# Performance work log

Measured on AMD Instinct MI355X. Metric: run time of the kernel, lower is better.

## Reference

```python
import itertools
import jax, jax.numpy as jnp
import numpy as np
from jax import lax

B, RES, C = 2048, 7, 512
N = RES * RES            # 49 tokens per window
HEADS = 4
KD = C // 16             # key_dim = 32
D = 4 * KD               # value dim = 128 == C // HEADS
KS = 5                   # dw-conv kernel
EPS = 1e-5


def _bias_idxs():
    pts = list(itertools.product(range(RES), range(RES)))
    offs, idxs = {}, []
    for p1 in pts:
        for p2 in pts:
            o = (abs(p1[0] - p2[0]), abs(p1[1] - p2[1]))
            if o not in offs:
                offs[o] = len(offs)
            idxs.append(offs[o])
    return np.array(idxs, np.int32).reshape(N, N), len(offs)


def setup_inputs() -> dict:
    key = jax.random.key(0)
    k = jax.random.split(key, 20)
    f = jnp.float32
    idxs, noff = _bias_idxs()  # noff == 49 for resolution 7
    qo = 2 * KD + D  # per-head qkv output channels = 192
    return {
        "x": jax.random.normal(k[0], (B, N, C), f),
        "qkv_w": jax.random.normal(k[1], (HEADS, qo, C // HEADS), f) * 0.05,
        "qkv_g": jnp.ones((HEADS, qo), f) + 0.1 * jax.random.normal(k[2], (HEADS, qo), f),
        "qkv_b": 0.1 * jax.random.normal(k[3], (HEADS, qo), f),
        "qkv_m": 0.1 * jax.random.normal(k[4], (HEADS, qo), f),
        "qkv_v": jax.random.uniform(k[5], (HEADS, qo), f, 0.5, 1.5),
        "dw_w": jax.random.normal(k[6], (HEADS, KD, 1, KS, KS), f) * 0.05,
        "dw_g": jnp.ones((HEADS, KD), f) + 0.1 * jax.random.normal(k[7], (HEADS, KD), f),
        "dw_b": 0.1 * jax.random.normal(k[8], (HEADS, KD), f),
        "dw_m": 0.1 * jax.random.normal(k[9], (HEADS, KD), f),
        "dw_v": jax.random.uniform(k[10], (HEADS, KD), f, 0.5, 1.5),
        "proj_w": jax.random.normal(k[11], (C, HEADS * D), f) * 0.05,
        "proj_g": jnp.ones((C,), f) + 0.1 * jax.random.normal(k[12], (C,), f),
        "proj_b": 0.1 * jax.random.normal(k[13], (C,), f),
        "proj_m": 0.1 * jax.random.normal(k[14], (C,), f),
        "proj_v": jax.random.uniform(k[15], (C,), f, 0.5, 1.5),
        "attn_bias": 0.1 * jax.random.normal(k[16], (HEADS, noff), f),
        "bias_idxs": jnp.asarray(idxs),
    }


def _bn(y, g, b, m, v):
    # inference-mode BatchNorm folded as per-channel affine (channels last)
    return (y - m) * (g * jax.lax.rsqrt(v + EPS)) + b


def reference(x, qkv_w, qkv_g, qkv_b, qkv_m, qkv_v,
              dw_w, dw_g, dw_b, dw_m, dw_v,
              proj_w, proj_g, proj_b, proj_m, proj_v,
              attn_bias, bias_idxs):
    scale = KD ** -0.5
    ab = attn_bias[:, bias_idxs]               # [HEADS, N, N] relative-position bias
    chunks = jnp.split(x, HEADS, axis=-1)      # per-head input chunks [B, N, C/HEADS]
    feat = chunks[0]
    outs = []
    for i in range(HEADS):
        if i > 0:
            feat = feat + chunks[i]            # cascade: prev head output + next chunk
        y = jnp.einsum('bnc,oc->bno', feat, qkv_w[i])
        y = _bn(y, qkv_g[i], qkv_b[i], qkv_m[i], qkv_v[i])   # [B, N, 192]
        q, k, v = y[..., :KD], y[..., KD:2 * KD], y[..., 2 * KD:]
        # depthwise 5x5 conv on q over the 7x7 window
        qi = q.reshape(B, RES, RES, KD)
        w = jnp.transpose(dw_w[i], (2, 3, 1, 0))  # OIHW(groups) -> HWIO [5,5,1,KD]
        qi = lax.conv_general_dilated(qi, w, (1, 1), 'SAME',
                                      feature_group_count=KD,
                                      dimension_numbers=('NHWC', 'HWIO', 'NHWC'))
        qi = _bn(qi, dw_g[i], dw_b[i], dw_m[i], dw_v[i])
        q = qi.reshape(B, N, KD)
        attn = jnp.einsum('bnk,bmk->bnm', q, k) * scale + ab[i]  # [B, N, N]
        attn = jax.nn.softmax(attn, axis=-1)
        feat = jnp.einsum('bnm,bmd->bnd', attn, v)               # [B, N, D]
        outs.append(feat)
    h = jax.nn.relu(jnp.concatenate(outs, axis=-1))              # [B, N, HEADS*D]
    out = jnp.einsum('bnd,od->bno', h, proj_w)
    out = _bn(out, proj_g, proj_b, proj_m, proj_v)               # [B, N, C]
    return out
```

## Files before the change

### kernel.cpp

```cpp
#include <hip/hip_runtime.h>
#include <hip/hip_bf16.h>

#define BATCH 2048
#define RES   7
#define NPOS  49
#define CDIM  512
#define HEADS 4
#define KD    32
#define DDIM  128
#define QO    192
#define EPS   1e-5f

#define FSTR 132
#define QSTR 36
#define ASTR 68
#define VSTR 72

#define OFF_QCV  0
#define OFF_ATT  7056
#define OFF_QBUF 25872
#define OFF_KBUF 32928
#define OFF_VTH  39984
#define OFF_VTL  58416
#define SMEM_SZ  76848

typedef __attribute__((ext_vector_type(8))) short short8;
typedef __attribute__((ext_vector_type(4))) float floatx4;

union S8u { short8 v; __hip_bfloat162 h[4]; };
union BU  { __hip_bfloat16 b; unsigned short u; };

__device__ inline short8 pack_bf16x8(float4 a, float4 b) {
    S8u u;
    u.h[0] = __float22bfloat162_rn(make_float2(a.x, a.y));
    u.h[1] = __float22bfloat162_rn(make_float2(a.z, a.w));
    u.h[2] = __float22bfloat162_rn(make_float2(b.x, b.y));
    u.h[3] = __float22bfloat162_rn(make_float2(b.z, b.w));
    return u.v;
}

__device__ inline void split_pack8(float4 a, float4 b, short8& hi, short8& lo) {
    S8u H, L;
    float v0[8] = {a.x, a.y, a.z, a.w, b.x, b.y, b.z, b.w};
    #pragma unroll
    for (int p = 0; p < 4; ++p) {
        __hip_bfloat162 hp = __float22bfloat162_rn(make_float2(v0[2*p], v0[2*p+1]));
        float h0 = __bfloat162float(hp.x);
        float h1 = __bfloat162float(hp.y);
        H.h[p] = hp;
        L.h[p] = __float22bfloat162_rn(make_float2(v0[2*p] - h0, v0[2*p+1] - h1));
    }
    hi = H.v; lo = L.v;
}

#define MFMA(a, b, c) __builtin_amdgcn_mfma_f32_16x16x32_bf16((a), (b), (c), 0, 0, 0)

__global__ __launch_bounds__(512, 2) void fused_cga_kernel(
    const float* __restrict__ x,
    const float* __restrict__ qkv_w,
    const float* __restrict__ qkv_g,  const float* __restrict__ qkv_bb,
    const float* __restrict__ qkv_m,  const float* __restrict__ qkv_v,
    const float* __restrict__ dw_w,
    const float* __restrict__ dw_g,   const float* __restrict__ dw_bb,
    const float* __restrict__ dw_m,   const float* __restrict__ dw_v,
    const float* __restrict__ proj_w,
    const float* __restrict__ proj_g, const float* __restrict__ proj_bb,
    const float* __restrict__ proj_m, const float* __restrict__ proj_v,
    const float* __restrict__ attn_bias,
    const int*   __restrict__ bias_idxs,
    float* __restrict__ out)
{
    __shared__ __align__(16) unsigned char smem[SMEM_SZ];
    float* feat = (float*)smem;
    float* qcv  = (float*)(smem + OFF_QCV);
    float* att  = (float*)(smem + OFF_ATT);
    float* qbuf = (float*)(smem + OFF_QBUF);
    float* kbuf = (float*)(smem + OFF_KBUF);
    unsigned short* vTh = (unsigned short*)(smem + OFF_VTH);
    unsigned short* vTl = (unsigned short*)(smem + OFF_VTL);

    const int b    = blockIdx.x;
    const int tid  = threadIdx.x;
    const int lane = tid & 63;
    const int wid  = tid >> 6;
    const int quad = lane >> 4;
    const int l15  = lane & 15;
    const int mt   = wid & 3;
    const int nh   = wid >> 2;

    const float* xb = x + (size_t)b * NPOS * CDIM;

    floatx4 po[16];
    #pragma unroll
    for (int t = 0; t < 16; ++t) po[t] = (floatx4){0.f, 0.f, 0.f, 0.f};

    for (int i = tid; i < 128 * 15; i += 512) {
        int d = i / 15, c = 49 + (i - d * 15);
        vTh[d * VSTR + c] = 0;
        vTl[d * VSTR + c] = 0;
    }

    for (int head = 0; head < HEADS; ++head) {
        for (int i = tid; i < NPOS * (DDIM / 4); i += 512) {
            int n = i >> 5, c4 = i & 31;
            float4 xv = *(const float4*)(xb + n * CDIM + head * DDIM + c4 * 4);
            float* fp = feat + n * FSTR + c4 * 4;
            if (head == 0) { *(float4*)fp = xv; }
            else {
                float4 f = *(float4*)fp;
                f.x += xv.x; f.y += xv.y; f.z += xv.z; f.w += xv.w;
                *(float4*)fp = f;
            }
        }
        __syncthreads();

        {
            floatx4 qa[6];
            #pragma unroll
            for (int t = 0; t < 6; ++t) qa[t] = (floatx4){0.f, 0.f, 0.f, 0.f};
            for (int ks = 0; ks < 4; ++ks) {
                const float* ap = feat + (mt * 16 + l15) * FSTR + ks * 32 + quad * 8;
                short8 ah, al;
                split_pack8(*(const float4*)ap, *(const float4*)(ap + 4), ah, al);
                #pragma unroll
                for (int t = 0; t < 6; ++t) {
                    const float* wp = qkv_w
                        + (size_t)(head * QO + nh * 96 + t * 16 + l15) * DDIM + ks * 32 + quad * 8;
                    short8 bh, bl;
                    split_pack8(*(const float4*)wp, *(const float4*)(wp + 4), bh, bl);
                    qa[t] = MFMA(ah, bh, qa[t]);
                    qa[t] = MFMA(al, bh, qa[t]);
                    qa[t] = MFMA(ah, bl, qa[t]);
                }
            }
            #pragma unroll
            for (int t = 0; t < 6; ++t) {
                int o   = nh * 96 + t * 16 + l15;
                int idx = head * QO + o;
                float s  = qkv_g[idx] * rsqrtf(qkv_v[idx] + EPS);
                float tt = qkv_bb[idx] - qkv_m[idx] * s;
                #pragma unroll
                for (int r = 0; r < 4; ++r) {
                    int row = mt * 16 + quad * 4 + r;
                    if (row < NPOS) {
                        float y = qa[t][r] * s + tt;
                        if (o < KD)          qbuf[row * QSTR + o] = y;
                        else if (o < 2 * KD) kbuf[row * QSTR + (o - KD)] = y;
                        else {
                            int d = o - 2 * KD;
                            BU hu, lu;
                            __hip_bfloat162 hp = __float22bfloat162_rn(make_float2(y, 0.f));
                            hu.b = hp.x;
                            float hf = __bfloat162float(hp.x);
                            __hip_bfloat162 lp = __float22bfloat162_rn(make_float2(y - hf, 0.f));
                            lu.b = lp.x;
                            vTh[d * VSTR + row] = hu.u;
                            vTl[d * VSTR + row] = lu.u;
                        }
                    }
                }
            }
        }
        __syncthreads();

        for (int i = tid; i < NPOS * KD; i += 512) {
            int n = i >> 5, ch = i & 31;
            int rr = n / RES, cc = n - rr * RES;
            const float* wd = dw_w + (size_t)(head * KD + ch) * 25;
            float acc = 0.f;
            #pragma unroll
            for (int dy = 0; dy < 5; ++dy) {
                int ry = rr + dy - 2;
                if (ry < 0 || ry >= RES) continue;
                #pragma unroll
                for (int dx = 0; dx < 5; ++dx) {
                    int cx = cc + dx - 2;
                    if (cx < 0 || cx >= RES) continue;
                    acc += qbuf[(ry * RES + cx) * QSTR + ch] * wd[dy * 5 + dx];
                }
            }
            int idx = head * KD + ch;
            float s  = dw_g[idx] * rsqrtf(dw_v[idx] + EPS);
            float tt = dw_bb[idx] - dw_m[idx] * s;
            qcv[n * QSTR + ch] = acc * s + tt;
        }
        __syncthreads();

        {
            floatx4 sa[2];
            sa[0] = (floatx4){0.f, 0.f, 0.f, 0.f};
            sa[1] = (floatx4){0.f, 0.f, 0.f, 0.f};
            const float* ap = qcv + (mt * 16 + l15) * QSTR + quad * 8;
            short8 ah, al;
            split_pack8(*(const float4*)ap, *(const float4*)(ap + 4), ah, al);
            #pragma unroll
            for (int t = 0; t < 2; ++t) {
                const float* kp = kbuf + ((nh * 2 + t) * 16 + l15) * QSTR + quad * 8;
                short8 bh, bl;
                split_pack8(*(const float4*)kp, *(const float4*)(kp + 4), bh, bl);
                sa[t] = MFMA(ah, bh, sa[t]);
                sa[t] = MFMA(al, bh, sa[t]);
                sa[t] = MFMA(ah, bl, sa[t]);
            }
            const float scale = 0.17677669529663687f;
            #pragma unroll
            for (int t = 0; t < 2; ++t) {
                int nn = (nh * 2 + t) * 16 + l15;
                #pragma unroll
                for (int r = 0; r < 4; ++r) {
                    int row = mt * 16 + quad * 4 + r;
                    if (row < NPOS) {
                        if (nn < NPOS)
                            att[row * ASTR + nn] = sa[t][r] * scale
                                + attn_bias[head * NPOS + bias_idxs[row * NPOS + nn]];
                        else
                            att[row * ASTR + nn] = 0.f;
                    }
                }
            }
        }
        __syncthreads();

        {
            int row = tid >> 3, g = tid & 7;
            if (row < NPOS) {
                float mx = -1e30f;
                for (int n = g; n < NPOS; n += 8) mx = fmaxf(mx, att[row * ASTR + n]);
                #pragma unroll
                for (int d = 1; d < 8; d <<= 1) mx = fmaxf(mx, __shfl_xor(mx, d));
                float sm = 0.f;
                for (int n = g; n < NPOS; n += 8) {
                    float e = __expf(att[row * ASTR + n] - mx);
                    att[row * ASTR + n] = e;
                    sm += e;
                }
                #pragma unroll
                for (int d = 1; d < 8; d <<= 1) sm += __shfl_xor(sm, d);
                float inv = 1.f / sm;
                for (int n = g; n < NPOS; n += 8) att[row * ASTR + n] *= inv;
            }
        }
        __syncthreads();

        {
            short8 ah[2], al[2];
            #pragma unroll
            for (int ks = 0; ks < 2; ++ks) {
                const float* ap = att + (mt * 16 + l15) * ASTR + ks * 32 + quad * 8;
                split_pack8(*(const float4*)ap, *(const float4*)(ap + 4), ah[ks], al[ks]);
            }
            __syncthreads();
            floatx4 pa[4];
            #pragma unroll
            for (int t = 0; t < 4; ++t) pa[t] = (floatx4){0.f, 0.f, 0.f, 0.f};
            #pragma unroll
            for (int ks = 0; ks < 2; ++ks) {
                #pragma unroll
                for (int t = 0; t < 4; ++t) {
                    int off = ((nh * 4 + t) * 16 + l15) * VSTR + ks * 32 + quad * 8;
                    short8 bh = *(const short8*)(vTh + off);
                    short8 bl = *(const short8*)(vTl + off);
                    pa[t] = MFMA(ah[ks], bh, pa[t]);
                    pa[t] = MFMA(al[ks], bh, pa[t]);
                    pa[t] = MFMA(ah[ks], bl, pa[t]);
                }
            }
            #pragma unroll
            for (int t = 0; t < 4; ++t) {
                int d = (nh * 4 + t) * 16 + l15;
                #pragma unroll
                for (int r = 0; r < 4; ++r) {
                    int row = mt * 16 + quad * 4 + r;
                    if (row < NPOS) feat[row * FSTR + d] = pa[t][r];
                }
            }
        }
        __syncthreads();

        {
            const int nbase = wid * 64;
            for (int ks = 0; ks < 4; ++ks) {
                short8 af[4];
                #pragma unroll
                for (int mm = 0; mm < 4; ++mm) {
                    const float* ap = feat + (mm * 16 + l15) * FSTR + ks * 32 + quad * 8;
                    float4 a0 = *(const float4*)ap;
                    float4 a1 = *(const float4*)(ap + 4);
                    a0.x = fmaxf(a0.x, 0.f); a0.y = fmaxf(a0.y, 0.f);
                    a0.z = fmaxf(a0.z, 0.f); a0.w = fmaxf(a0.w, 0.f);
                    a1.x = fmaxf(a1.x, 0.f); a1.y = fmaxf(a1.y, 0.f);
                    a1.z = fmaxf(a1.z, 0.f); a1.w = fmaxf(a1.w, 0.f);
                    af[mm] = pack_bf16x8(a0, a1);
                }
                #pragma unroll
                for (int j = 0; j < 4; ++j) {
                    const float* wp = proj_w
                        + (size_t)(nbase + j * 16 + l15) * CDIM + head * DDIM + ks * 32 + quad * 8;
                    short8 bf = pack_bf16x8(*(const float4*)wp, *(const float4*)(wp + 4));
                    #pragma unroll
                    for (int mm = 0; mm < 4; ++mm)
                        po[mm * 4 + j] = MFMA(af[mm], bf, po[mm * 4 + j]);
                }
            }
        }
        __syncthreads();
    }

    {
        const int nbase = wid * 64;
        #pragma unroll
        for (int j = 0; j < 4; ++j) {
            int o = nbase + j * 16 + l15;
            float s  = proj_g[o] * rsqrtf(proj_v[o] + EPS);
            float tt = proj_bb[o] - proj_m[o] * s;
            #pragma unroll
            for (int mm = 0; mm < 4; ++mm) {
                #pragma unroll
                for (int r = 0; r < 4; ++r) {
                    int row = mm * 16 + quad * 4 + r;
                    if (row < NPOS)
                        out[((size_t)b * NPOS + row) * CDIM + o] = po[mm * 4 + j][r] * s + tt;
                }
            }
        }
    }
}

extern "C" void kernel_launch(void* const* d_in, const int* in_sizes, int n_in,
                              void* d_out, int out_size, void* d_ws, size_t ws_size,
                              hipStream_t stream) {
    const float* x      = (const float*)d_in[0];
    const float* qkv_w  = (const float*)d_in[1];
    const float* qkv_g  = (const float*)d_in[2];
    const float* qkv_b  = (const float*)d_in[3];
    const float* qkv_m  = (const float*)d_in[4];
    const float* qkv_v  = (const float*)d_in[5];
    const float* dw_w   = (const float*)d_in[6];
    const float* dw_g   = (const float*)d_in[7];
    const float* dw_b   = (const float*)d_in[8];
    const float* dw_m   = (const float*)d_in[9];
    const float* dw_v   = (const float*)d_in[10];
    const float* proj_w = (const float*)d_in[11];
    const float* proj_g = (const float*)d_in[12];
    const float* proj_b = (const float*)d_in[13];
    const float* proj_m = (const float*)d_in[14];
    const float* proj_v = (const float*)d_in[15];
    const float* attn_bias = (const float*)d_in[16];
    const int*   bias_idxs = (const int*)d_in[17];
    float* out = (float*)d_out;
    (void)d_ws; (void)ws_size;

    hipLaunchKernelGGL(fused_cga_kernel, dim3(BATCH), dim3(512), 0, stream,
        x, qkv_w, qkv_g, qkv_b, qkv_m, qkv_v,
        dw_w, dw_g, dw_b, dw_m, dw_v,
        proj_w, proj_g, proj_b, proj_m, proj_v,
        attn_bias, bias_idxs, out);
}
```

Measured before the change: 1.429 ms.

## Split fused kernel into attention and projection kernels via bf16 staging in output

Removes the per-head projection accumulation, along with its 16 floatx4 register accumulators, from the attention kernel. Each head's ReLU'd output is written as bf16 into the output buffer as scratch, and a second kernel runs the full K=512 projection plus BatchNorm from shared memory. Launch bounds rise from 2 to 4 blocks per CU to take advantage of the lower register pressure. In exchange it adds a global write and read of the intermediate and a second launch, and the 76.8KB of LDS per block may cap occupancy below the new launch bound.

```diff
diff --git a/kernel.cpp b/kernel.cpp
--- a/kernel.cpp
+++ b/kernel.cpp
@@ -23,6 +23,8 @@
 #define OFF_VTH  39984
 #define OFF_VTL  58416
 #define SMEM_SZ  76848
+
+#define HSTR 520
 
 typedef __attribute__((ext_vector_type(8))) short short8;
 typedef __attribute__((ext_vector_type(4))) float floatx4;
@@ -55,7 +57,7 @@
 
 #define MFMA(a, b, c) __builtin_amdgcn_mfma_f32_16x16x32_bf16((a), (b), (c), 0, 0, 0)
 
-__global__ __launch_bounds__(512, 2) void fused_cga_kernel(
+__global__ __launch_bounds__(512, 4) void cga_attn_kernel(
     const float* __restrict__ x,
     const float* __restrict__ qkv_w,
     const float* __restrict__ qkv_g,  const float* __restrict__ qkv_bb,
@@ -63,9 +65,6 @@
     const float* __restrict__ dw_w,
     const float* __restrict__ dw_g,   const float* __restrict__ dw_bb,
     const float* __restrict__ dw_m,   const float* __restrict__ dw_v,
-    const float* __restrict__ proj_w,
-    const float* __restrict__ proj_g, const float* __restrict__ proj_bb,
-    const float* __restrict__ proj_m, const float* __restrict__ proj_v,
     const float* __restrict__ attn_bias,
     const int*   __restrict__ bias_idxs,
     float* __restrict__ out)
@@ -89,10 +88,7 @@
     const int nh   = wid >> 2;
 
     const float* xb = x + (size_t)b * NPOS * CDIM;
-
-    floatx4 po[16];
-    #pragma unroll
-    for (int t = 0; t < 16; ++t) po[t] = (floatx4){0.f, 0.f, 0.f, 0.f};
+    unsigned short* hb = (unsigned short*)(out + (size_t)b * NPOS * CDIM);
 
     for (int i = tid; i < 128 * 15; i += 512) {
         int d = i / 15, c = 49 + (i - d * 15);
@@ -271,56 +267,80 @@
                 #pragma unroll
                 for (int r = 0; r < 4; ++r) {
                     int row = mt * 16 + quad * 4 + r;
-                    if (row < NPOS) feat[row * FSTR + d] = pa[t][r];
-                }
-            }
-        }
-        __syncthreads();
-
-        {
-            const int nbase = wid * 64;
-            for (int ks = 0; ks < 4; ++ks) {
-                short8 af[4];
-                #pragma unroll
-                for (int mm = 0; mm < 4; ++mm) {
-                    const float* ap = feat + (mm * 16 + l15) * FSTR + ks * 32 + quad * 8;
-                    float4 a0 = *(const float4*)ap;
-                    float4 a1 = *(const float4*)(ap + 4);
-                    a0.x = fmaxf(a0.x, 0.f); a0.y = fmaxf(a0.y, 0.f);
-                    a0.z = fmaxf(a0.z, 0.f); a0.w = fmaxf(a0.w, 0.f);
-                    a1.x = fmaxf(a1.x, 0.f); a1.y = fmaxf(a1.y, 0.f);
-                    a1.z = fmaxf(a1.z, 0.f); a1.w = fmaxf(a1.w, 0.f);
-                    af[mm] = pack_bf16x8(a0, a1);
-                }
-                #pragma unroll
-                for (int j = 0; j < 4; ++j) {
-                    const float* wp = proj_w
-                        + (size_t)(nbase + j * 16 + l15) * CDIM + head * DDIM + ks * 32 + quad * 8;
-                    short8 bf = pack_bf16x8(*(const float4*)wp, *(const float4*)(wp + 4));
-                    #pragma unroll
-                    for (int mm = 0; mm < 4; ++mm)
-                        po[mm * 4 + j] = MFMA(af[mm], bf, po[mm * 4 + j]);
-                }
-            }
-        }
-        __syncthreads();
-    }
-
-    {
-        const int nbase = wid * 64;
+                    if (row < NPOS) {
+                        feat[row * FSTR + d] = pa[t][r];
+                        __hip_bfloat162 hp =
+                            __float22bfloat162_rn(make_float2(fmaxf(pa[t][r], 0.f), 0.f));
+                        BU u; u.b = hp.x;
+                        hb[row * CDIM + head * DDIM + d] = u.u;
+                    }
+                }
+            }
+        }
+        __syncthreads();
+    }
+}
+
+__global__ __launch_bounds__(512, 4) void proj_kernel(
+    const float* __restrict__ pw,
+    const float* __restrict__ proj_g, const float* __restrict__ proj_bb,
+    const float* __restrict__ proj_m, const float* __restrict__ proj_v,
+    float* __restrict__ io)
+{
+    __shared__ __align__(16) unsigned short hs[64 * HSTR];
+
+    const int b   = blockIdx.x;
+    const int tid = threadIdx.x;
+    float* iob = io + (size_t)b * NPOS * CDIM;
+    const unsigned short* hsrc = (const unsigned short*)iob;
+
+    for (int i = tid; i < NPOS * 64; i += 512) {
+        int row = i >> 6, c8 = i & 63;
+        *(short8*)(hs + row * HSTR + c8 * 8) = *(const short8*)(hsrc + row * 512 + c8 * 8);
+    }
+    for (int i = tid; i < 15 * 64; i += 512) {
+        int row = 49 + (i >> 6), c8 = i & 63;
+        *(short8*)(hs + row * HSTR + c8 * 8) = (short8){0,0,0,0,0,0,0,0};
+    }
+    __syncthreads();
+
+    const int lane  = tid & 63;
+    const int wid   = tid >> 6;
+    const int quad  = lane >> 4;
+    const int l15   = lane & 15;
+    const int nbase = wid * 64;
+
+    floatx4 po[16];
+    #pragma unroll
+    for (int t = 0; t < 16; ++t) po[t] = (floatx4){0.f, 0.f, 0.f, 0.f};
+
+    for (int ks = 0; ks < 16; ++ks) {
+        short8 af[4];
+        #pragma unroll
+        for (int mm = 0; mm < 4; ++mm)
+            af[mm] = *(const short8*)(hs + (mm * 16 + l15) * HSTR + ks * 32 + quad * 8);
         #pragma unroll
         for (int j = 0; j < 4; ++j) {
-            int o = nbase + j * 16 + l15;
-            float s  = proj_g[o] * rsqrtf(proj_v[o] + EPS);
-            float tt = proj_bb[o] - proj_m[o] * s;
-            #pragma unroll
-            for (int mm = 0; mm < 4; ++mm) {
-                #pragma unroll
-                for (int r = 0; r < 4; ++r) {
-                    int row = mm * 16 + quad * 4 + r;
-                    if (row < NPOS)
-                        out[((size_t)b * NPOS + row) * CDIM + o] = po[mm * 4 + j][r] * s + tt;
-                }
+            const float* wp = pw + (size_t)(nbase + j * 16 + l15) * CDIM + ks * 32 + quad * 8;
+            short8 bf = pack_bf16x8(*(const float4*)wp, *(const float4*)(wp + 4));
+            #pragma unroll
+            for (int mm = 0; mm < 4; ++mm)
+                po[mm * 4 + j] = MFMA(af[mm], bf, po[mm * 4 + j]);
+        }
+    }
+
+    #pragma unroll
+    for (int j = 0; j < 4; ++j) {
+        int o = nbase + j * 16 + l15;
+        float s  = proj_g[o] * rsqrtf(proj_v[o] + EPS);
+        float tt = proj_bb[o] - proj_m[o] * s;
+        #pragma unroll
+        for (int mm = 0; mm < 4; ++mm) {
+            #pragma unroll
+            for (int r = 0; r < 4; ++r) {
+                int row = mm * 16 + quad * 4 + r;
+                if (row < NPOS)
+                    iob[(size_t)row * CDIM + o] = po[mm * 4 + j][r] * s + tt;
             }
         }
     }
@@ -350,9 +370,10 @@
     float* out = (float*)d_out;
     (void)d_ws; (void)ws_size;
 
-    hipLaunchKernelGGL(fused_cga_kernel, dim3(BATCH), dim3(512), 0, stream,
+    hipLaunchKernelGGL(cga_attn_kernel, dim3(BATCH), dim3(512), 0, stream,
         x, qkv_w, qkv_g, qkv_b, qkv_m, qkv_v,
         dw_w, dw_g, dw_b, dw_m, dw_v,
-        proj_w, proj_g, proj_b, proj_m, proj_v,
         attn_bias, bias_idxs, out);
-}
+    hipLaunchKernelGGL(proj_kernel, dim3(BATCH), dim3(512), 0, stream,
+        proj_w, proj_g, proj_b, proj_m, proj_v, out);
+}
```

New measurement: 1.277 ms. 10.7% less time.
